# Kernel tuning notes

Measured on AMD Instinct MI355X. Metric: run time of the kernel, lower is better.

Reference implementation:

```python
import jax, jax.numpy as jnp
import numpy as np


def setup_inputs() -> dict:
    key = jax.random.key(0)
    B, D, C, H = 4096, 64, 128, 512
    ks = jax.random.split(key, 6)
    return {
        "q_z_x_params": jax.random.normal(ks[0], (B, C), jnp.float32),
        "eps": jax.random.normal(ks[1], (B, D), jnp.float32),
        "W1": jax.random.normal(ks[2], (D + C, H), jnp.float32) / np.sqrt(D + C).astype(np.float32),
        "b1": jnp.zeros((H,), jnp.float32),
        "W2": jax.random.normal(ks[3], (H, H), jnp.float32) / np.sqrt(H).astype(np.float32),
        "b2": jnp.zeros((H,), jnp.float32),
        "W3": jax.random.normal(ks[4], (H, 2 * D), jnp.float32) / np.sqrt(H).astype(np.float32),
        "b3": jnp.zeros((2 * D,), jnp.float32),
    }


def _made_masks(D, C, H):
    # Standard MADE degrees, natural ordering; context columns fully connected.
    m_in = np.arange(1, D + 1)                      # input degrees 1..D
    m_h = (np.arange(H) % (D - 1)) + 1              # hidden degrees 1..D-1
    M1 = np.concatenate([m_h[None, :] >= m_in[:, None],
                         np.ones((C, H), bool)], axis=0)   # (D+C, H)
    M2 = m_h[None, :] >= m_h[:, None]               # (H, H)
    m_out = np.tile(np.arange(1, D + 1), 2)         # (2D,) mean||prescale
    M3 = m_out[None, :] > m_h[:, None]              # (H, 2D)
    f32 = jnp.float32
    return jnp.asarray(M1, f32), jnp.asarray(M2, f32), jnp.asarray(M3, f32)


def reference(q_z_x_params, eps, W1, b1, W2, b2, W3, b3):
    B, D = eps.shape
    C = q_z_x_params.shape[1]
    H = W2.shape[0]
    M1, M2, M3 = _made_masks(D, C, H)
    mW1, mW2, mW3 = W1 * M1, W2 * M2, W3 * M3

    def made(z):
        x = jnp.concatenate([z, q_z_x_params], axis=1)   # (B, D+C)
        h1 = jax.nn.relu(x @ mW1 + b1)
        h2 = jax.nn.relu(h1 @ mW2 + b2)
        out = h2 @ mW3 + b3                              # (B, 2D)
        return out[:, :D], out[:, D:]

    def step(z, i):
        mean, prescale = made(z)
        mu_i = jnp.take(mean, i, axis=1)                 # (B,)
        scale_i = jax.nn.softplus(jnp.take(prescale, i, axis=1))
        z_i = mu_i + scale_i * jnp.take(eps, i, axis=1)  # reparameterized Normal sample
        z = z.at[:, i].set(z_i)
        return z, None

    z0 = jnp.zeros((B, D), eps.dtype)
    z_sample, _ = jax.lax.scan(step, z0, jnp.arange(D))
    return z_sample
```

## Files before the change

### kernel.cpp

```cpp
#include <hip/hip_runtime.h>
#include <math.h>

#define DD 64
#define CC 128
#define HH 512
#define BATCH 4096

typedef __attribute__((ext_vector_type(2))) float f32x2;

__device__ __forceinline__ f32x2 splat2(float x) { f32x2 v; v[0] = x; v[1] = x; return v; }

__device__ __forceinline__ f32x2 pk_fma(f32x2 a, f32x2 b, f32x2 c) {
    f32x2 d;
    asm("v_pk_fma_f32 %0, %1, %2, %3" : "=v"(d) : "v"(a), "v"(b), "v"(c));
    return d;
}

__device__ __forceinline__ float fast_softplus(float x) {
    float t = exp2f(-fabsf(x) * 1.44269504f);
    return fmaxf(x, 0.f) + 0.69314718f * log2f(1.f + t);
}

__device__ __forceinline__ float bcast(float x, int l) {
    return __int_as_float(__builtin_amdgcn_readlane(__float_as_int(x), l));
}

typedef const __attribute__((address_space(1))) void* as1_cptr;
typedef __attribute__((address_space(3))) void* as3_ptr;
__device__ __forceinline__ void glds16(const float* g, float* l) {
    __builtin_amdgcn_global_load_lds((as1_cptr)g, (as3_ptr)l, 16, 0, 0);
}

__global__ __launch_bounds__(256, 2) void made_sample(
    const float* __restrict__ ctx,
    const float* __restrict__ eps,
    const float* __restrict__ W1,
    const float* __restrict__ b1,
    const float* __restrict__ W2,
    const float* __restrict__ b2,
    const float* __restrict__ W3,
    const float* __restrict__ b3,
    float* __restrict__ out)
{
    const int lane  = threadIdx.x & 63;
    const int w     = threadIdx.x >> 6;
    const int rbase = blockIdx.x * 8 + w * 2;
    const int jbase = 8 * lane;

    __shared__ float sbuf[2][10 * HH];
    __shared__ float w3sb[2][5 * 256];

    int deg[8];
    #pragma unroll
    for (int u = 0; u < 8; ++u) deg[u] = (jbase + u) % 63 + 1;

    auto load8v = [&](const float* base_, f32x2* r_) {
        float4 a = *(const float4*)(base_ + lane * 4);
        float4 b = *(const float4*)(base_ + 256 + lane * 4);
        r_[0][0] = a.x; r_[0][1] = a.y; r_[1][0] = a.z; r_[1][1] = a.w;
        r_[2][0] = b.x; r_[2][1] = b.y; r_[3][0] = b.z; r_[3][1] = b.w;
    };
    auto stage_row = [&](const float* src, float* dst) {
        glds16(src + lane * 8,     dst);
        glds16(src + lane * 8 + 4, dst + 256);
    };
    auto stage_w3pair = [&](int k0, int k1, float* dst) {
        const float* g = (lane < 32) ? (W3 + k0 * (2 * DD) + lane * 4)
                                     : (W3 + k1 * (2 * DD) + (lane - 32) * 4);
        glds16(g, dst);
    };

    f32x2 p1[2][4], p2[2][4], acc[2];
    #pragma unroll
    for (int j = 0; j < 4; ++j) {
        f32x2 t1, t2;
        t1[0] = b1[jbase + 2 * j]; t1[1] = b1[jbase + 2 * j + 1];
        t2[0] = b2[jbase + 2 * j]; t2[1] = b2[jbase + 2 * j + 1];
        p1[0][j] = t1; p1[1][j] = t1;
        p2[0][j] = t2; p2[1][j] = t2;
    }
    acc[0] = splat2(0.f);
    acc[1] = splat2(0.f);

    float ca[2], cb[2], ep[2];
    #pragma unroll
    for (int r = 0; r < 2; ++r) {
        ca[r] = ctx[(rbase + r) * CC + lane];
        cb[r] = ctx[(rbase + r) * CC + 64 + lane];
        ep[r] = eps[(rbase + r) * DD + lane];
    }
    const float b3m = b3[lane];
    const float b3p = b3[64 + lane];

    auto stage_ctx = [&](int ch, float* buf) {
        #pragma unroll
        for (int q2 = 0; q2 < 2; ++q2) {
            const int q = 2 * w + q2;
            stage_row(W1 + (DD + 8 * ch + q) * HH, buf + q * HH);
        }
    };
    auto stage_step = [&](int in, float* buf, float* w3buf) {
        if (in == 0) {
            if (w == 1) stage_row(W1, buf + 9 * HH);
            return;
        }
        const int basen = in - 1;
        const bool h9n = basen < 8;
        stage_row(W2 + (basen + 63 * w) * HH,       buf + w * HH);
        stage_row(W2 + (basen + 63 * (4 + w)) * HH, buf + (4 + w) * HH);
        if (w == 1) stage_row(W1 + in * HH, buf + 9 * HH);
        if (w == 0 && h9n) {
            stage_row(W2 + (basen + 504) * HH, buf + 8 * HH);
            stage_w3pair(basen + 504, basen + 504, w3buf + 4 * 256);
        }
        if (w >= 2) {
            #pragma unroll
            for (int pp = 0; pp < 2; ++pp) {
                const int p = 2 * (w - 2) + pp;
                stage_w3pair(basen + 63 * (2 * p), basen + 63 * (2 * p + 1),
                             w3buf + p * 256);
            }
        }
    };

    stage_ctx(0, sbuf[0]);
    __syncthreads();
    #pragma unroll 1
    for (int ch = 0; ch < 16; ++ch) {
        float* cur = sbuf[ch & 1];
        f32x2 cw[8][4];
        #pragma unroll
        for (int q = 0; q < 8; ++q) load8v(cur + q * HH, cw[q]);
        if (ch < 15) stage_ctx(ch + 1, sbuf[(ch + 1) & 1]);
        else         stage_step(0, sbuf[0], w3sb[0]);
        #pragma unroll
        for (int q = 0; q < 8; ++q) {
            const int c = 8 * ch + q;
            #pragma unroll
            for (int r = 0; r < 2; ++r) {
                const float cv = bcast((ch < 8) ? ca[r] : cb[r], c & 63);
                const f32x2 cv2 = splat2(cv);
                #pragma unroll
                for (int j = 0; j < 4; ++j) p1[r][j] = pk_fma(cv2, cw[q][j], p1[r][j]);
            }
        }
        __syncthreads();
    }

    float z[2] = {0.f, 0.f};

    #pragma unroll 1
    for (int i = 0; i < DD; ++i) {
        float* cur = sbuf[i & 1];
        const float* w3s = w3sb[i & 1];

        f32x2 w1v[4];
        load8v(cur + 9 * HH, w1v);
        f32x2 wv[9][4];
        float wa[9], wb[9];
        if (i > 0) {
            #pragma unroll
            for (int t = 0; t < 9; ++t) load8v(cur + t * HH, wv[t]);
            #pragma unroll
            for (int t = 0; t < 9; ++t) {
                wa[t] = w3s[t * 128 + lane];
                wb[t] = w3s[t * 128 + 64 + lane];
            }
        }

        if (i < 63) stage_step(i + 1, sbuf[(i + 1) & 1], w3sb[(i + 1) & 1]);

        if (i > 0) {
            const int base = i - 1;
            const bool h9 = base < 8;

            float m0 = 0.f, m1 = 0.f;
            #pragma unroll
            for (int u = 0; u < 8; ++u) {
                const bool e = (deg[u] == i);
                m0 = e ? p1[0][u >> 1][u & 1] : m0;
                m1 = e ? p1[1][u >> 1][u & 1] : m1;
            }
            m0 = fmaxf(m0, 0.f);
            m1 = fmaxf(m1, 0.f);

            #pragma unroll
            for (int t = 0; t < 8; ++t) {
                const int k = base + 63 * t;
                const f32x2 h0 = splat2(bcast(m0, k >> 3));
                const f32x2 h1 = splat2(bcast(m1, k >> 3));
                #pragma unroll
                for (int j = 0; j < 4; ++j) {
                    p2[0][j] = pk_fma(h0, wv[t][j], p2[0][j]);
                    p2[1][j] = pk_fma(h1, wv[t][j], p2[1][j]);
                }
            }
            if (h9) {
                const f32x2 h0 = splat2(bcast(m0, 63));
                const f32x2 h1 = splat2(bcast(m1, 63));
                #pragma unroll
                for (int j = 0; j < 4; ++j) {
                    p2[0][j] = pk_fma(h0, wv[8][j], p2[0][j]);
                    p2[1][j] = pk_fma(h1, wv[8][j], p2[1][j]);
                }
            }

            float g0 = 0.f, g1 = 0.f;
            #pragma unroll
            for (int u = 0; u < 8; ++u) {
                const bool e = (deg[u] == i);
                g0 = e ? p2[0][u >> 1][u & 1] : g0;
                g1 = e ? p2[1][u >> 1][u & 1] : g1;
            }
            g0 = fmaxf(g0, 0.f);
            g1 = fmaxf(g1, 0.f);

            #pragma unroll
            for (int t = 0; t < 8; ++t) {
                const int k = base + 63 * t;
                const float h0 = bcast(g0, k >> 3);
                const float h1 = bcast(g1, k >> 3);
                acc[0][0] = fmaf(h0, wa[t], acc[0][0]);
                acc[0][1] = fmaf(h0, wb[t], acc[0][1]);
                acc[1][0] = fmaf(h1, wa[t], acc[1][0]);
                acc[1][1] = fmaf(h1, wb[t], acc[1][1]);
            }
            if (h9) {
                const float h0 = bcast(g0, 63);
                const float h1 = bcast(g1, 63);
                acc[0][0] = fmaf(h0, wa[8], acc[0][0]);
                acc[0][1] = fmaf(h0, wb[8], acc[0][1]);
                acc[1][0] = fmaf(h1, wa[8], acc[1][0]);
                acc[1][1] = fmaf(h1, wb[8], acc[1][1]);
            }
        }

        {
            #pragma unroll
            for (int r = 0; r < 2; ++r) {
                const float am = acc[r][0] + b3m;
                const float ap = acc[r][1] + b3p;
                const float sp = fast_softplus(ap);
                const float zc = fmaf(sp, ep[r], am);
                const float zi = bcast(zc, i);
                if (lane == i) z[r] = zi;
                const f32x2 zi2 = splat2(zi);
                #pragma unroll
                for (int j = 0; j < 4; ++j) p1[r][j] = pk_fma(zi2, w1v[j], p1[r][j]);
            }
        }

        __syncthreads();
    }

    #pragma unroll
    for (int r = 0; r < 2; ++r) out[(rbase + r) * DD + lane] = z[r];
}

extern "C" void kernel_launch(void* const* d_in, const int* in_sizes, int n_in,
                              void* d_out, int out_size, void* d_ws, size_t ws_size,
                              hipStream_t stream) {
    const float* ctx = (const float*)d_in[0];
    const float* eps = (const float*)d_in[1];
    const float* W1  = (const float*)d_in[2];
    const float* b1  = (const float*)d_in[3];
    const float* W2  = (const float*)d_in[4];
    const float* b2  = (const float*)d_in[5];
    const float* W3  = (const float*)d_in[6];
    const float* b3  = (const float*)d_in[7];
    (void)d_ws; (void)ws_size; (void)in_sizes; (void)n_in; (void)out_size;

    made_sample<<<BATCH / 8, 256, 0, stream>>>(ctx, eps, W1, b1, W2, b2, W3, b3,
                                               (float*)d_out);
}
```

Baseline: 179.7 us.

## Double block to 8 waves sharing staged weights; feed packed FMA from SGPR pairs

Each block now runs 8 waves over 16 rows, so every weight row staged into LDS serves twice as many batch rows. Staging is redistributed so each wave loads one W2 row per step, and W3 pair loads are spread over waves 2-6. Broadcast hidden values now go straight from readlane into an SGPR pair used as the packed-FMA operand, which removes the VGPR splat moves. Async staging is issued before the LDS reads, with a sched_barrier after them. The risk is fewer resident blocks per CU from the larger block size and register pressure, and the block count drops to 256, which may underfill the GPU's CUs.

Measured after the change: 197.4 us. +9.9%, slower.

```diff
diff --git a/kernel.cpp b/kernel.cpp
--- a/kernel.cpp
+++ b/kernel.cpp
@@ -7,6 +7,7 @@
 #define BATCH 4096
 
 typedef __attribute__((ext_vector_type(2))) float f32x2;
+typedef unsigned long long u64;
 
 __device__ __forceinline__ f32x2 splat2(float x) { f32x2 v; v[0] = x; v[1] = x; return v; }
 
@@ -15,6 +16,11 @@
     asm("v_pk_fma_f32 %0, %1, %2, %3" : "=v"(d) : "v"(a), "v"(b), "v"(c));
     return d;
 }
+__device__ __forceinline__ f32x2 pk_fma_s(u64 hpair, f32x2 b, f32x2 c) {
+    f32x2 d;
+    asm("v_pk_fma_f32 %0, %1, %2, %3" : "=v"(d) : "s"(hpair), "v"(b), "v"(c));
+    return d;
+}
 
 __device__ __forceinline__ float fast_softplus(float x) {
     float t = exp2f(-fabsf(x) * 1.44269504f);
@@ -23,6 +29,10 @@
 
 __device__ __forceinline__ float bcast(float x, int l) {
     return __int_as_float(__builtin_amdgcn_readlane(__float_as_int(x), l));
+}
+__device__ __forceinline__ u64 rl_pair(float x, int l) {
+    unsigned u = (unsigned)__builtin_amdgcn_readlane(__float_as_int(x), l);
+    return ((u64)u << 32) | u;
 }
 
 typedef const __attribute__((address_space(1))) void* as1_cptr;
@@ -31,7 +41,7 @@
     __builtin_amdgcn_global_load_lds((as1_cptr)g, (as3_ptr)l, 16, 0, 0);
 }
 
-__global__ __launch_bounds__(256, 2) void made_sample(
+__global__ __launch_bounds__(512, 2) void made_sample(
     const float* __restrict__ ctx,
     const float* __restrict__ eps,
     const float* __restrict__ W1,
@@ -44,7 +54,7 @@
 {
     const int lane  = threadIdx.x & 63;
     const int w     = threadIdx.x >> 6;
-    const int rbase = blockIdx.x * 8 + w * 2;
+    const int rbase = blockIdx.x * 16 + w * 2;
     const int jbase = 8 * lane;
 
     __shared__ float sbuf[2][10 * HH];
@@ -93,11 +103,7 @@
     const float b3p = b3[64 + lane];
 
     auto stage_ctx = [&](int ch, float* buf) {
-        #pragma unroll
-        for (int q2 = 0; q2 < 2; ++q2) {
-            const int q = 2 * w + q2;
-            stage_row(W1 + (DD + 8 * ch + q) * HH, buf + q * HH);
-        }
+        stage_row(W1 + (DD + 8 * ch + w) * HH, buf + w * HH);
     };
     auto stage_step = [&](int in, float* buf, float* w3buf) {
         if (in == 0) {
@@ -106,21 +112,16 @@
         }
         const int basen = in - 1;
         const bool h9n = basen < 8;
-        stage_row(W2 + (basen + 63 * w) * HH,       buf + w * HH);
-        stage_row(W2 + (basen + 63 * (4 + w)) * HH, buf + (4 + w) * HH);
+        stage_row(W2 + (basen + 63 * w) * HH, buf + w * HH);
+        if (w == 0 && h9n) stage_row(W2 + (basen + 504) * HH, buf + 8 * HH);
         if (w == 1) stage_row(W1 + in * HH, buf + 9 * HH);
-        if (w == 0 && h9n) {
-            stage_row(W2 + (basen + 504) * HH, buf + 8 * HH);
+        if (w >= 2 && w <= 5) {
+            const int p = w - 2;
+            stage_w3pair(basen + 63 * (2 * p), basen + 63 * (2 * p + 1),
+                         w3buf + p * 256);
+        }
+        if (w == 6 && h9n)
             stage_w3pair(basen + 504, basen + 504, w3buf + 4 * 256);
-        }
-        if (w >= 2) {
-            #pragma unroll
-            for (int pp = 0; pp < 2; ++pp) {
-                const int p = 2 * (w - 2) + pp;
-                stage_w3pair(basen + 63 * (2 * p), basen + 63 * (2 * p + 1),
-                             w3buf + p * 256);
-            }
-        }
     };
 
     stage_ctx(0, sbuf[0]);
@@ -128,20 +129,20 @@
     #pragma unroll 1
     for (int ch = 0; ch < 16; ++ch) {
         float* cur = sbuf[ch & 1];
+        if (ch < 15) stage_ctx(ch + 1, sbuf[(ch + 1) & 1]);
+        else         stage_step(0, sbuf[0], w3sb[0]);
         f32x2 cw[8][4];
         #pragma unroll
         for (int q = 0; q < 8; ++q) load8v(cur + q * HH, cw[q]);
-        if (ch < 15) stage_ctx(ch + 1, sbuf[(ch + 1) & 1]);
-        else         stage_step(0, sbuf[0], w3sb[0]);
+        __builtin_amdgcn_sched_barrier(0);
         #pragma unroll
         for (int q = 0; q < 8; ++q) {
             const int c = 8 * ch + q;
             #pragma unroll
             for (int r = 0; r < 2; ++r) {
-                const float cv = bcast((ch < 8) ? ca[r] : cb[r], c & 63);
-                const f32x2 cv2 = splat2(cv);
-                #pragma unroll
-                for (int j = 0; j < 4; ++j) p1[r][j] = pk_fma(cv2, cw[q][j], p1[r][j]);
+                const u64 cvp = rl_pair((ch < 8) ? ca[r] : cb[r], c & 63);
+                #pragma unroll
+                for (int j = 0; j < 4; ++j) p1[r][j] = pk_fma_s(cvp, cw[q][j], p1[r][j]);
             }
         }
         __syncthreads();
@@ -153,6 +154,8 @@
     for (int i = 0; i < DD; ++i) {
         float* cur = sbuf[i & 1];
         const float* w3s = w3sb[i & 1];
+
+        if (i < 63) stage_step(i + 1, sbuf[(i + 1) & 1], w3sb[(i + 1) & 1]);
 
         f32x2 w1v[4];
         load8v(cur + 9 * HH, w1v);
@@ -167,8 +170,7 @@
                 wb[t] = w3s[t * 128 + 64 + lane];
             }
         }
-
-        if (i < 63) stage_step(i + 1, sbuf[(i + 1) & 1], w3sb[(i + 1) & 1]);
+        __builtin_amdgcn_sched_barrier(0);
 
         if (i > 0) {
             const int base = i - 1;
@@ -187,21 +189,21 @@
             #pragma unroll
             for (int t = 0; t < 8; ++t) {
                 const int k = base + 63 * t;
-                const f32x2 h0 = splat2(bcast(m0, k >> 3));
-                const f32x2 h1 = splat2(bcast(m1, k >> 3));
+                const u64 h0 = rl_pair(m0, k >> 3);
+                const u64 h1 = rl_pair(m1, k >> 3);
                 #pragma unroll
                 for (int j = 0; j < 4; ++j) {
-                    p2[0][j] = pk_fma(h0, wv[t][j], p2[0][j]);
-                    p2[1][j] = pk_fma(h1, wv[t][j], p2[1][j]);
+                    p2[0][j] = pk_fma_s(h0, wv[t][j], p2[0][j]);
+                    p2[1][j] = pk_fma_s(h1, wv[t][j], p2[1][j]);
                 }
             }
             if (h9) {
-                const f32x2 h0 = splat2(bcast(m0, 63));
-                const f32x2 h1 = splat2(bcast(m1, 63));
+                const u64 h0 = rl_pair(m0, 63);
+                const u64 h1 = rl_pair(m1, 63);
                 #pragma unroll
                 for (int j = 0; j < 4; ++j) {
-                    p2[0][j] = pk_fma(h0, wv[8][j], p2[0][j]);
-                    p2[1][j] = pk_fma(h1, wv[8][j], p2[1][j]);
+                    p2[0][j] = pk_fma_s(h0, wv[8][j], p2[0][j]);
+                    p2[1][j] = pk_fma_s(h1, wv[8][j], p2[1][j]);
                 }
             }
 
@@ -244,9 +246,9 @@
                 const float zc = fmaf(sp, ep[r], am);
                 const float zi = bcast(zc, i);
                 if (lane == i) z[r] = zi;
-                const f32x2 zi2 = splat2(zi);
-                #pragma unroll
-                for (int j = 0; j < 4; ++j) p1[r][j] = pk_fma(zi2, w1v[j], p1[r][j]);
+                const u64 zp = rl_pair(zc, i);
+                #pragma unroll
+                for (int j = 0; j < 4; ++j) p1[r][j] = pk_fma_s(zp, w1v[j], p1[r][j]);
             }
         }
 
@@ -270,6 +272,6 @@
     const float* b3  = (const float*)d_in[7];
     (void)d_ws; (void)ws_size; (void)in_sizes; (void)n_in; (void)out_size;
 
-    made_sample<<<BATCH / 8, 256, 0, stream>>>(ctx, eps, W1, b1, W2, b2, W3, b3,
-                                               (float*)d_out);
-}
+    made_sample<<<BATCH / 16, 512, 0, stream>>>(ctx, eps, W1, b1, W2, b2, W3, b3,
+                                                (float*)d_out);
+}
```
